# Kernel tuning notes

Measured on AMD Instinct MI355X. Metric: run time of the kernel, lower is better.

Reference implementation:

```python
import jax, jax.numpy as jnp
import numpy as np
import itertools

# ---- module constants (mirroring HyperLayer init) ----
B = 16          # batchsize
K = 16384       # number of learned index tuples (k)
ADD = 32        # additional sampled integer tuples per point
RANK = 2        # len(learn_cols) = w_rank; learn_cols = (0, 1)
P = 2 ** RANK + ADD  # candidate integer tuples per real-valued point
IN_DIM = 65536
OUT_DIM = 65536
EPSILON = 1e-6
SIGMA_BOOST = 2.0

# floor/ceil mask: rows of itertools.product([True, False], repeat=RANK) -> (2^RANK, RANK)
_FLOOR_MASK = jnp.array(
    [[int(b) for b in bools] for bools in itertools.product([True, False], repeat=RANK)],
    dtype=bool,
)


def setup_inputs() -> dict:
    key = jax.random.key(0)
    k1, k2, k3, k4 = jax.random.split(key, 4)
    return {
        "x": jax.random.normal(k1, (B, IN_DIM), jnp.float32),
        "res": jax.random.normal(k2, (B, K, RANK + 2), jnp.float32),
        "bias": jax.random.normal(k3, (OUT_DIM,), jnp.float32),
        "temp_indices": jax.random.randint(k4, (K, 2), 0, IN_DIM, dtype=jnp.int64),
    }


def _forward(x, res, bias, temp_indices):
    bsz = x.shape[0]
    # subrange = [out_size, in_size] for learn_cols = (0, 1)
    size = jnp.array([OUT_DIM, IN_DIM], jnp.float32)

    # ---- split_out: means in [0, size-1], sigmas softplus-scaled by size ----
    means = jax.nn.sigmoid(res[..., :RANK]) * (size - 1.0)               # (B, K, 2)
    sigmas = (jax.nn.softplus(res[..., RANK] + SIGMA_BOOST) + EPSILON)[..., None] * size  # (B, K, 2)
    values = res[..., RANK + 1]                                          # (B, K)

    # ---- discretize: 2^RANK floor/ceil neighbors (on detached means) ----
    m_det = jax.lax.stop_gradient(means)[:, :, None, :]                  # (B, K, 1, 2)
    nb = jnp.where(_FLOOR_MASK[None, None], jnp.floor(m_det), jnp.ceil(m_det)).astype(jnp.int32)  # (B,K,4,2)

    # additional uniformly sampled integer tuples (fixed internal key, deterministic)
    u = jax.random.uniform(jax.random.key(42), (bsz, K, ADD, RANK), jnp.float32) * (1.0 - EPSILON)
    samp = jnp.floor(u * size).astype(jnp.int32)                         # (B, K, ADD, 2)

    ints = jnp.concatenate([nb, samp], axis=2)                           # (B, K, P, 2)
    ints_fl = ints.astype(jnp.float32)

    # diagonal-Gaussian densities of integer tuples under (means, sigmas)
    z = (ints_fl - means[:, :, None, :]) / sigmas[:, :, None, :]         # (B, K, P, 2)
    props = jnp.exp(-0.5 * jnp.sum(z * z, axis=-1))                      # (B, K, P)
    props = props / jnp.sum(props + EPSILON, axis=2, keepdims=True)

    vals = (values[:, :, None] * props).reshape(bsz, -1)                 # (B, L)
    idx = ints.reshape(bsz, -1, RANK)                                    # (B, L, 2)

    # template: hardwired temp_indices, with learn_cols overwritten by discretized indices
    template = jnp.broadcast_to(
        temp_indices.astype(jnp.int32)[None, :, None, :], (bsz, K, P, 2)
    ).reshape(bsz, -1, 2)
    template = template.at[:, :, jnp.array([0, 1])].set(idx)

    out_idx = template[..., 0]                                           # (B, L) in [0, OUT_DIM)
    in_idx = template[..., 1]                                            # (B, L) in [0, IN_DIM)

    # sparse matrix-vector product per batch element: gather then scatter-add
    gathered = jnp.take_along_axis(x, in_idx, axis=1)                    # (B, L)
    contrib = vals * gathered                                            # (B, L)
    flat = (jnp.arange(bsz, dtype=jnp.int32)[:, None] * OUT_DIM + out_idx).reshape(-1)
    y = jnp.zeros((bsz * OUT_DIM,), x.dtype).at[flat].add(contrib.reshape(-1))
    return y.reshape(bsz, OUT_DIM) + bias[None, :]


def reference(x, res, bias, temp_indices):
    return _forward(x, res, bias, temp_indices)
```

## Files before the change

### kernel.cpp

```cpp
#include <hip/hip_runtime.h>
#include <stdint.h>
#include <math.h>

#define NB 16
#define NK 16384
#define NADD 32
#define NP 36
#define DIM 65536

#define TPB 512
#define GPB2 32
#define NCH3 4
#define CHW3 16384

typedef float f32x4 __attribute__((ext_vector_type(4)));
typedef float f32x8 __attribute__((ext_vector_type(8)));
typedef unsigned int u32x2 __attribute__((ext_vector_type(2)));
typedef unsigned int u32x4 __attribute__((ext_vector_type(4)));

#define BAR_LGKM() asm volatile("s_waitcnt lgkmcnt(0)\n\ts_barrier" ::: "memory")

__device__ __forceinline__ uint32_t rotl32(uint32_t x, uint32_t r) {
    return (x << r) | (x >> (32u - r));
}

__device__ __forceinline__ uint32_t tf_bits(uint32_t idx) {
    const uint32_t K1 = 42u;
    const uint32_t K2 = 0x1BD11BDAu ^ 42u;
    uint32_t x0 = 0u;
    uint32_t x1 = idx + K1;
#define TF_ROUND(r) { x0 += x1; x1 = rotl32(x1, r); x1 ^= x0; }
#define TF_G(a,b,c,d) TF_ROUND(a) TF_ROUND(b) TF_ROUND(c) TF_ROUND(d)
    TF_G(13,15,26,6)   x0 += K1;  x1 += K2 + 1u;
    TF_G(17,29,16,24)  x0 += K2;  x1 += 2u;
    TF_G(13,15,26,6)              x1 += K1 + 3u;
    TF_G(17,29,16,24)  x0 += K1;  x1 += K2 + 4u;
    TF_G(13,15,26,6)   x0 += K2;  x1 += 5u;
#undef TF_G
#undef TF_ROUND
    return x0 ^ x1;
}

__device__ __forceinline__ void tf_bits4(uint32_t base,
                                         uint32_t& r0, uint32_t& r1,
                                         uint32_t& r2, uint32_t& r3) {
    const uint32_t K1 = 42u;
    const uint32_t K2 = 0x1BD11BDAu ^ 42u;
    uint32_t x0[4] = {0u, 0u, 0u, 0u};
    uint32_t x1[4] = {base + K1, base + 1u + K1, base + 2u + K1, base + 3u + K1};
#define TFR4(r) { \
    x0[0]+=x1[0]; x1[0]=rotl32(x1[0],r); x1[0]^=x0[0]; \
    x0[1]+=x1[1]; x1[1]=rotl32(x1[1],r); x1[1]^=x0[1]; \
    x0[2]+=x1[2]; x1[2]=rotl32(x1[2],r); x1[2]^=x0[2]; \
    x0[3]+=x1[3]; x1[3]=rotl32(x1[3],r); x1[3]^=x0[3]; }
#define TFG4(a,b,c,d) TFR4(a) TFR4(b) TFR4(c) TFR4(d)
#define INJ4(da, db) { \
    x0[0]+=(da); x1[0]+=(db); x0[1]+=(da); x1[1]+=(db); \
    x0[2]+=(da); x1[2]+=(db); x0[3]+=(da); x1[3]+=(db); }
    TFG4(13,15,26,6)   INJ4(K1, K2 + 1u)
    TFG4(17,29,16,24)  INJ4(K2, 2u)
    TFG4(13,15,26,6)   INJ4(0u, K1 + 3u)
    TFG4(17,29,16,24)  INJ4(K1, K2 + 4u)
    TFG4(13,15,26,6)   INJ4(K2, 5u)
#undef TFR4
#undef TFG4
#undef INJ4
    r0 = x0[0] ^ x1[0];
    r1 = x0[1] ^ x1[1];
    r2 = x0[2] ^ x1[2];
    r3 = x0[3] ^ x1[3];
}

__device__ __forceinline__ float xla_expf(float x0) {
    float x = fminf(fmaxf(x0, -88.3762626647949f), 88.3762626647950f);
    const float fx = floorf(__fadd_rn(__fmul_rn(x, 1.44269504088896341f), 0.5f));
    const float tmp = __fmul_rn(fx, 0.693359375f);
    float z = __fmul_rn(fx, -2.12194440e-4f);
    float r = __fsub_rn(x, tmp);
    r = __fsub_rn(r, z);
    z = __fmul_rn(r, r);
    float y = 1.9875691500E-4f;
    y = __fadd_rn(__fmul_rn(y, r), 1.3981999507E-3f);
    y = __fadd_rn(__fmul_rn(y, r), 8.3334519073E-3f);
    y = __fadd_rn(__fmul_rn(y, r), 4.1665795894E-2f);
    y = __fadd_rn(__fmul_rn(y, r), 1.6666665459E-1f);
    y = __fadd_rn(__fmul_rn(y, r), 5.0000001201E-1f);
    y = __fadd_rn(__fmul_rn(y, z), r);
    y = __fadd_rn(y, 1.0f);
    const int n = (int)fx;
    const float p2n = __uint_as_float((uint32_t)(n + 127) << 23);
    return fmaxf(__fmul_rn(y, p2n), x0);
}

__device__ __forceinline__ uint32_t bf16pair(float a, float b) {
    uint32_t ua = __float_as_uint(a), ub = __float_as_uint(b);
    ua = (ua + 0x7FFFu + ((ua >> 16) & 1u)) >> 16;
    ub = (ub + 0x7FFFu + ((ub >> 16) & 1u)) >> 16;
    return ua | (ub << 16);
}


__global__ __launch_bounds__(TPB, 4) void f1_gen_reduce_bf16(
    const float*  __restrict__ x,
    const float4* __restrict__ res4,
    uint32_t* __restrict__ part)
{
    __shared__ float acc[CHW3];
    f32x4* const acc4 = reinterpret_cast<f32x4*>(acc);
    const int blk = blockIdx.x;
    const uint32_t tid = (uint32_t)blk * TPB + threadIdx.x;
    const int b = (int)(tid >> 14);
    const float* __restrict__ xrow = x + ((size_t)b << 16);

    #pragma unroll
    for (int j = 0; j < 8; ++j)
        acc4[j * TPB + threadIdx.x] = (f32x4)(0.0f);

    const float4 r = res4[tid];

    const float e0 = xla_expf(-r.x);
    const float e1 = xla_expf(-r.y);
    const float s0 = __fdiv_rn(1.0f, __fadd_rn(1.0f, e0));
    const float s1 = __fdiv_rn(1.0f, __fadd_rn(1.0f, e1));
    const float m0 = __fmul_rn(s0, 65535.0f);
    const float m1 = __fmul_rn(s1, 65535.0f);

    const float a2 = r.z + 2.0f;
    const float sp = fmaxf(a2, 0.0f) + log1pf(__expf(-fabsf(a2)));
    const float sigma = (sp + 1e-6f) * 65536.0f;
    const float inv_sig = __builtin_amdgcn_rcpf(sigma);
    const float n2 = -0.5f * inv_sig * inv_sig;
    const float val = r.w;

    uint32_t packed[NP];
    float    xv[NP];

    {
        const float f0 = floorf(m0), c0 = ceilf(m0);
        const float f1v = floorf(m1), c1 = ceilf(m1);
        const uint32_t uf0 = (uint32_t)(int)f0, uc0 = (uint32_t)(int)c0;
        const uint32_t uf1 = (uint32_t)(int)f1v, uc1 = (uint32_t)(int)c1;
        packed[0] = (uf0 << 16) | uf1;  xv[0] = xrow[uf1];
        packed[1] = (uf0 << 16) | uc1;  xv[1] = xrow[uc1];
        packed[2] = (uc0 << 16) | uf1;  xv[2] = xrow[uf1];
        packed[3] = (uc0 << 16) | uc1;  xv[3] = xrow[uc1];
    }

    const float ONE_MEPS = (float)(1.0 - 1e-6);
    const uint32_t base = tid * 64u;
    #pragma unroll
    for (int a = 0; a < NADD; a += 2) {
        uint32_t bb0, bb1, bb2, bb3;
        tf_bits4(base + 2u*(uint32_t)a, bb0, bb1, bb2, bb3);
        const float u0a = __fmul_rn(__uint_as_float((bb0 >> 9) | 0x3f800000u) - 1.0f, ONE_MEPS);
        const float u1a = __fmul_rn(__uint_as_float((bb1 >> 9) | 0x3f800000u) - 1.0f, ONE_MEPS);
        const float s0a = floorf(__fmul_rn(u0a, 65536.0f));
        const float s1a = floorf(__fmul_rn(u1a, 65536.0f));
        const uint32_t pa = ((uint32_t)(int)s0a << 16) | (uint32_t)(int)s1a;
        packed[4 + a] = pa;
        xv[4 + a] = xrow[pa & 0xFFFFu];
        const float u0b = __fmul_rn(__uint_as_float((bb2 >> 9) | 0x3f800000u) - 1.0f, ONE_MEPS);
        const float u1b = __fmul_rn(__uint_as_float((bb3 >> 9) | 0x3f800000u) - 1.0f, ONE_MEPS);
        const float s0b = floorf(__fmul_rn(u0b, 65536.0f));
        const float s1b = floorf(__fmul_rn(u1b, 65536.0f));
        const uint32_t pb = ((uint32_t)(int)s0b << 16) | (uint32_t)(int)s1b;
        packed[5 + a] = pb;
        xv[5 + a] = xrow[pb & 0xFFFFu];
    }

    float w[NP];
    float denom = 0.0f;
    #pragma unroll
    for (int p = 0; p < NP; ++p) {
        const float d0 = (float)(int)(packed[p] >> 16) - m0;
        const float d1 = (float)(int)(packed[p] & 0xFFFFu) - m1;
        const float e = __expf(n2 * fmaf(d1, d1, d0 * d0));
        denom += e + 1e-6f;
        w[p] = e * xv[p];
    }
    const float scale = __fdiv_rn(val, denom);
    #pragma unroll
    for (int p = 0; p < NP; ++p) w[p] *= scale;

    __syncthreads();

    uint32_t* __restrict__ dst = part + ((size_t)blk << 15);
    #pragma unroll 1
    for (uint32_t c = 0; c < NCH3; ++c) {
        #pragma unroll
        for (int p = 0; p < NP; ++p) {
            if ((packed[p] >> 30) == c)
                atomicAdd(&acc[(packed[p] >> 16) & (CHW3 - 1)], w[p]);
        }
        BAR_LGKM();
        u32x2* __restrict__ dst2 =
            reinterpret_cast<u32x2*>(dst + (size_t)c * 8192);
        const bool last = (c == NCH3 - 1);
        #pragma unroll
        for (int j = 0; j < 8; ++j) {
            const int idx = j * TPB + (int)threadIdx.x;
            const f32x4 v = acc4[idx];
            const u32x2 o = { bf16pair(v.x, v.y), bf16pair(v.z, v.w) };
            dst2[idx] = o;
            if (!last) acc4[idx] = (f32x4)(0.0f);
        }
        if (!last) BAR_LGKM();
    }
}

__global__ __launch_bounds__(256) void f2_final_bf16(
    const u32x4* __restrict__ part4,
    const f32x8* __restrict__ bias8,
    f32x8* __restrict__ y8)
{
    const int i = blockIdx.x * 256 + threadIdx.x;
    const int o8 = i & 8191;
    const int b = i >> 13;
    f32x8 s = bias8[o8];
    #pragma unroll
    for (int g = 0; g < GPB2; ++g) {
        const u32x4 p = part4[(((size_t)(b * GPB2 + g)) << 13) + o8];
        s[0] += __uint_as_float(p.x << 16);
        s[1] += __uint_as_float(p.x & 0xFFFF0000u);
        s[2] += __uint_as_float(p.y << 16);
        s[3] += __uint_as_float(p.y & 0xFFFF0000u);
        s[4] += __uint_as_float(p.z << 16);
        s[5] += __uint_as_float(p.z & 0xFFFF0000u);
        s[6] += __uint_as_float(p.w << 16);
        s[7] += __uint_as_float(p.w & 0xFFFF0000u);
    }
    __builtin_nontemporal_store(s, &y8[i]);
}


__device__ __forceinline__ void gen_point(const float4 r, uint32_t tid,
                                          uint32_t* packed, float* w) {
    const float e0 = xla_expf(-r.x);
    const float e1 = xla_expf(-r.y);
    const float s0 = __fdiv_rn(1.0f, __fadd_rn(1.0f, e0));
    const float s1 = __fdiv_rn(1.0f, __fadd_rn(1.0f, e1));
    const float m0 = __fmul_rn(s0, 65535.0f);
    const float m1 = __fmul_rn(s1, 65535.0f);
    const float a2 = r.z + 2.0f;
    const float sp = fmaxf(a2, 0.0f) + log1pf(__expf(-fabsf(a2)));
    const float sigma = (sp + 1e-6f) * 65536.0f;
    const float inv_sig = __builtin_amdgcn_rcpf(sigma);
    const float n2 = -0.5f * inv_sig * inv_sig;
    const float val = r.w;

    const float f0 = floorf(m0), c0 = ceilf(m0);
    const float f1 = floorf(m1), c1 = ceilf(m1);
    {
        const float cd0[4] = {f0, f0, c0, c0};
        const float cd1[4] = {f1, c1, f1, c1};
        #pragma unroll
        for (int p = 0; p < 4; ++p) {
            const float d0 = cd0[p] - m0;
            const float d1 = cd1[p] - m1;
            w[p] = __expf(n2 * fmaf(d1, d1, d0 * d0));
            packed[p] = ((uint32_t)(int)cd0[p] << 16) | (uint32_t)(int)cd1[p];
        }
    }
    const float ONE_MEPS = (float)(1.0 - 1e-6);
    const uint32_t base = tid * 64u;
    #pragma unroll
    for (int a = 0; a < NADD; ++a) {
        const uint32_t bb0 = tf_bits(base + 2u*(uint32_t)a);
        const uint32_t bb1 = tf_bits(base + 2u*(uint32_t)a + 1u);
        const float u0 = __fmul_rn(__uint_as_float((bb0 >> 9) | 0x3f800000u) - 1.0f, ONE_MEPS);
        const float u1 = __fmul_rn(__uint_as_float((bb1 >> 9) | 0x3f800000u) - 1.0f, ONE_MEPS);
        const float s0f = floorf(__fmul_rn(u0, 65536.0f));
        const float s1f = floorf(__fmul_rn(u1, 65536.0f));
        const float d0 = s0f - m0;
        const float d1 = s1f - m1;
        w[4 + a] = __expf(n2 * fmaf(d1, d1, d0 * d0));
        packed[4 + a] = ((uint32_t)(int)s0f << 16) | (uint32_t)(int)s1f;
    }
    float denom = 0.0f;
    #pragma unroll
    for (int p = 0; p < NP; ++p) denom += w[p] + 1e-6f;
    const float scale = __fdiv_rn(val, denom);
    #pragma unroll
    for (int p = 0; p < NP; ++p) w[p] *= scale;
}

__global__ __launch_bounds__(256) void init_bias_kernel(
    const float4* __restrict__ bias4, float4* __restrict__ y4)
{
    const int i = blockIdx.x * 256 + threadIdx.x;
    y4[i] = bias4[i & 16383];
}

__global__ __launch_bounds__(256) void hyper_scatter(
    const float*  __restrict__ x,
    const float4* __restrict__ res4,
    float*        __restrict__ y)
{
    const int tid = blockIdx.x * 256 + threadIdx.x;
    const int b = tid >> 14;
    uint32_t packed[NP];
    float    w[NP];
    gen_point(res4[tid], (uint32_t)tid, packed, w);
    const float* __restrict__ xrow = x + ((size_t)b << 16);
    float*       __restrict__ yrow = y + ((size_t)b << 16);
    #pragma unroll
    for (int p = 0; p < NP; ++p) {
        const float xv = xrow[packed[p] & 0xFFFFu];
        unsafeAtomicAdd(&yrow[packed[p] >> 16], w[p] * xv);
    }
}

extern "C" void kernel_launch(void* const* d_in, const int* in_sizes, int n_in,
                              void* d_out, int out_size, void* d_ws, size_t ws_size,
                              hipStream_t stream) {
    const float*  x     = (const float*)d_in[0];
    const float4* res4  = (const float4*)d_in[1];
    const float4* bias4 = (const float4*)d_in[2];
    float* y = (float*)d_out;

    const size_t need_bf16 = (size_t)NB * GPB2 * DIM * 2;

    if (ws_size >= need_bf16) {
        uint32_t* part = (uint32_t*)d_ws;
        f1_gen_reduce_bf16<<<NB * GPB2, TPB, 0, stream>>>(x, res4, part);
        f2_final_bf16<<<(NB * DIM / 8) / 256, 256, 0, stream>>>(
            (const u32x4*)part, (const f32x8*)bias4, (f32x8*)y);
    } else {
        init_bias_kernel<<<(NB * DIM / 4) / 256, 256, 0, stream>>>(bias4, (float4*)y);
        hyper_scatter<<<(NB * NK) / 256, 256, 0, stream>>>(x, res4, y);
    }
}
```

Measured before the change: 153.5 us.

## Replace LDS-chunked bf16 partial reduction with direct global float atomics

Removes the two-pass scheme, where each block accumulated into shared memory chunks, wrote bf16 partials to workspace and a second kernel summed them with bias. It uses a bias-init kernel followed by a scatter kernel. The scatter kernel reuses the precomputed weighted x values and issues 36 unsafe float atomics per point straight into the output. This drops the large partial-buffer write and read and the bf16 rounding. The cost is heavy global atomic contention across 16K points per batch row.

```diff
diff --git a/kernel.cpp b/kernel.cpp
--- a/kernel.cpp
+++ b/kernel.cpp
@@ -8,17 +8,8 @@
 #define NP 36
 #define DIM 65536
 
-#define TPB 512
-#define GPB2 32
-#define NCH3 4
-#define CHW3 16384
 
 typedef float f32x4 __attribute__((ext_vector_type(4)));
-typedef float f32x8 __attribute__((ext_vector_type(8)));
-typedef unsigned int u32x2 __attribute__((ext_vector_type(2)));
-typedef unsigned int u32x4 __attribute__((ext_vector_type(4)));
-
-#define BAR_LGKM() asm volatile("s_waitcnt lgkmcnt(0)\n\ts_barrier" ::: "memory")
 
 __device__ __forceinline__ uint32_t rotl32(uint32_t x, uint32_t r) {
     return (x << r) | (x >> (32u - r));
@@ -92,29 +83,23 @@
     return fmaxf(__fmul_rn(y, p2n), x0);
 }
 
-__device__ __forceinline__ uint32_t bf16pair(float a, float b) {
-    uint32_t ua = __float_as_uint(a), ub = __float_as_uint(b);
-    ua = (ua + 0x7FFFu + ((ua >> 16) & 1u)) >> 16;
-    ub = (ub + 0x7FFFu + ((ub >> 16) & 1u)) >> 16;
-    return ua | (ub << 16);
+
+__global__ __launch_bounds__(256) void init_bias_kernel(
+    const float4* __restrict__ bias4, float4* __restrict__ y4)
+{
+    const int i = blockIdx.x * 256 + threadIdx.x;
+    y4[i] = bias4[i & 16383];
 }
 
-
-__global__ __launch_bounds__(TPB, 4) void f1_gen_reduce_bf16(
+__global__ __launch_bounds__(256) void hyper_scatter_opt(
     const float*  __restrict__ x,
     const float4* __restrict__ res4,
-    uint32_t* __restrict__ part)
+    float*        __restrict__ y)
 {
-    __shared__ float acc[CHW3];
-    f32x4* const acc4 = reinterpret_cast<f32x4*>(acc);
-    const int blk = blockIdx.x;
-    const uint32_t tid = (uint32_t)blk * TPB + threadIdx.x;
+    const uint32_t tid = (uint32_t)blockIdx.x * 256u + threadIdx.x;
     const int b = (int)(tid >> 14);
     const float* __restrict__ xrow = x + ((size_t)b << 16);
-
-    #pragma unroll
-    for (int j = 0; j < 8; ++j)
-        acc4[j * TPB + threadIdx.x] = (f32x4)(0.0f);
+    float*       __restrict__ yrow = y + ((size_t)b << 16);
 
     const float4 r = res4[tid];
 
@@ -179,134 +164,10 @@
         w[p] = e * xv[p];
     }
     const float scale = __fdiv_rn(val, denom);
-    #pragma unroll
-    for (int p = 0; p < NP; ++p) w[p] *= scale;
 
-    __syncthreads();
-
-    uint32_t* __restrict__ dst = part + ((size_t)blk << 15);
-    #pragma unroll 1
-    for (uint32_t c = 0; c < NCH3; ++c) {
-        #pragma unroll
-        for (int p = 0; p < NP; ++p) {
-            if ((packed[p] >> 30) == c)
-                atomicAdd(&acc[(packed[p] >> 16) & (CHW3 - 1)], w[p]);
-        }
-        BAR_LGKM();
-        u32x2* __restrict__ dst2 =
-            reinterpret_cast<u32x2*>(dst + (size_t)c * 8192);
-        const bool last = (c == NCH3 - 1);
-        #pragma unroll
-        for (int j = 0; j < 8; ++j) {
-            const int idx = j * TPB + (int)threadIdx.x;
-            const f32x4 v = acc4[idx];
-            const u32x2 o = { bf16pair(v.x, v.y), bf16pair(v.z, v.w) };
-            dst2[idx] = o;
-            if (!last) acc4[idx] = (f32x4)(0.0f);
-        }
-        if (!last) BAR_LGKM();
-    }
-}
-
-__global__ __launch_bounds__(256) void f2_final_bf16(
-    const u32x4* __restrict__ part4,
-    const f32x8* __restrict__ bias8,
-    f32x8* __restrict__ y8)
-{
-    const int i = blockIdx.x * 256 + threadIdx.x;
-    const int o8 = i & 8191;
-    const int b = i >> 13;
-    f32x8 s = bias8[o8];
-    #pragma unroll
-    for (int g = 0; g < GPB2; ++g) {
-        const u32x4 p = part4[(((size_t)(b * GPB2 + g)) << 13) + o8];
-        s[0] += __uint_as_float(p.x << 16);
-        s[1] += __uint_as_float(p.x & 0xFFFF0000u);
-        s[2] += __uint_as_float(p.y << 16);
-        s[3] += __uint_as_float(p.y & 0xFFFF0000u);
-        s[4] += __uint_as_float(p.z << 16);
-        s[5] += __uint_as_float(p.z & 0xFFFF0000u);
-        s[6] += __uint_as_float(p.w << 16);
-        s[7] += __uint_as_float(p.w & 0xFFFF0000u);
-    }
-    __builtin_nontemporal_store(s, &y8[i]);
-}
-
-
-__device__ __forceinline__ void gen_point(const float4 r, uint32_t tid,
-                                          uint32_t* packed, float* w) {
-    const float e0 = xla_expf(-r.x);
-    const float e1 = xla_expf(-r.y);
-    const float s0 = __fdiv_rn(1.0f, __fadd_rn(1.0f, e0));
-    const float s1 = __fdiv_rn(1.0f, __fadd_rn(1.0f, e1));
-    const float m0 = __fmul_rn(s0, 65535.0f);
-    const float m1 = __fmul_rn(s1, 65535.0f);
-    const float a2 = r.z + 2.0f;
-    const float sp = fmaxf(a2, 0.0f) + log1pf(__expf(-fabsf(a2)));
-    const float sigma = (sp + 1e-6f) * 65536.0f;
-    const float inv_sig = __builtin_amdgcn_rcpf(sigma);
-    const float n2 = -0.5f * inv_sig * inv_sig;
-    const float val = r.w;
-
-    const float f0 = floorf(m0), c0 = ceilf(m0);
-    const float f1 = floorf(m1), c1 = ceilf(m1);
-    {
-        const float cd0[4] = {f0, f0, c0, c0};
-        const float cd1[4] = {f1, c1, f1, c1};
-        #pragma unroll
-        for (int p = 0; p < 4; ++p) {
-            const float d0 = cd0[p] - m0;
-            const float d1 = cd1[p] - m1;
-            w[p] = __expf(n2 * fmaf(d1, d1, d0 * d0));
-            packed[p] = ((uint32_t)(int)cd0[p] << 16) | (uint32_t)(int)cd1[p];
-        }
-    }
-    const float ONE_MEPS = (float)(1.0 - 1e-6);
-    const uint32_t base = tid * 64u;
-    #pragma unroll
-    for (int a = 0; a < NADD; ++a) {
-        const uint32_t bb0 = tf_bits(base + 2u*(uint32_t)a);
-        const uint32_t bb1 = tf_bits(base + 2u*(uint32_t)a + 1u);
-        const float u0 = __fmul_rn(__uint_as_float((bb0 >> 9) | 0x3f800000u) - 1.0f, ONE_MEPS);
-        const float u1 = __fmul_rn(__uint_as_float((bb1 >> 9) | 0x3f800000u) - 1.0f, ONE_MEPS);
-        const float s0f = floorf(__fmul_rn(u0, 65536.0f));
-        const float s1f = floorf(__fmul_rn(u1, 65536.0f));
-        const float d0 = s0f - m0;
-        const float d1 = s1f - m1;
-        w[4 + a] = __expf(n2 * fmaf(d1, d1, d0 * d0));
-        packed[4 + a] = ((uint32_t)(int)s0f << 16) | (uint32_t)(int)s1f;
-    }
-    float denom = 0.0f;
-    #pragma unroll
-    for (int p = 0; p < NP; ++p) denom += w[p] + 1e-6f;
-    const float scale = __fdiv_rn(val, denom);
-    #pragma unroll
-    for (int p = 0; p < NP; ++p) w[p] *= scale;
-}
-
-__global__ __launch_bounds__(256) void init_bias_kernel(
-    const float4* __restrict__ bias4, float4* __restrict__ y4)
-{
-    const int i = blockIdx.x * 256 + threadIdx.x;
-    y4[i] = bias4[i & 16383];
-}
-
-__global__ __launch_bounds__(256) void hyper_scatter(
-    const float*  __restrict__ x,
-    const float4* __restrict__ res4,
-    float*        __restrict__ y)
-{
-    const int tid = blockIdx.x * 256 + threadIdx.x;
-    const int b = tid >> 14;
-    uint32_t packed[NP];
-    float    w[NP];
-    gen_point(res4[tid], (uint32_t)tid, packed, w);
-    const float* __restrict__ xrow = x + ((size_t)b << 16);
-    float*       __restrict__ yrow = y + ((size_t)b << 16);
     #pragma unroll
     for (int p = 0; p < NP; ++p) {
-        const float xv = xrow[packed[p] & 0xFFFFu];
-        unsafeAtomicAdd(&yrow[packed[p] >> 16], w[p] * xv);
+        unsafeAtomicAdd(&yrow[packed[p] >> 16], w[p] * scale);
     }
 }
 
@@ -318,15 +179,9 @@
     const float4* bias4 = (const float4*)d_in[2];
     float* y = (float*)d_out;
 
-    const size_t need_bf16 = (size_t)NB * GPB2 * DIM * 2;
+    (void)d_ws; (void)ws_size;
 
-    if (ws_size >= need_bf16) {
-        uint32_t* part = (uint32_t*)d_ws;
-        f1_gen_reduce_bf16<<<NB * GPB2, TPB, 0, stream>>>(x, res4, part);
-        f2_final_bf16<<<(NB * DIM / 8) / 256, 256, 0, stream>>>(
-            (const u32x4*)part, (const f32x8*)bias4, (f32x8*)y);
-    } else {
-        init_bias_kernel<<<(NB * DIM / 4) / 256, 256, 0, stream>>>(bias4, (float4*)y);
-        hyper_scatter<<<(NB * NK) / 256, 256, 0, stream>>>(x, res4, y);
-    }
+    init_bias_kernel<<<(NB * DIM / 4) / 256, 256, 0, stream>>>(
+        bias4, (float4*)y);
+    hyper_scatter_opt<<<(NB * NK) / 256, 256, 0, stream>>>(x, res4, y);
 }
```

Measured after the change: 529.9 us. +245.1%, slower.

## Split each point's candidates across two threads with shuffle-combined denominator

Applied to the files above, without the earlier changes.

Each real-valued point is now handled by a pair of threads: both compute the shared sigmoid/softplus terms, one also handles the four floor/ceil neighbours, and each generates and processes 16 of the 32 sampled tuples. The two partial softmax denominators are combined with a lane shuffle. Blocks grow to 1024 threads while still covering 512 points, so the shared-memory chunk clears and flushes take half as many iterations per thread. This cuts per-thread register arrays and the serial Threefry/exp chain to raise parallelism, at the cost of duplicated prologue math, divergence between the two halves, and larger blocks.

```diff
diff --git a/kernel.cpp b/kernel.cpp
--- a/kernel.cpp
+++ b/kernel.cpp
@@ -8,10 +8,12 @@
 #define NP 36
 #define DIM 65536
 
-#define TPB 512
+#define TPB 1024
+#define PPB 512
 #define GPB2 32
 #define NCH3 4
 #define CHW3 16384
+#define NSPT 16
 
 typedef float f32x4 __attribute__((ext_vector_type(4)));
 typedef float f32x8 __attribute__((ext_vector_type(8)));
@@ -108,15 +110,16 @@
     __shared__ float acc[CHW3];
     f32x4* const acc4 = reinterpret_cast<f32x4*>(acc);
     const int blk = blockIdx.x;
-    const uint32_t tid = (uint32_t)blk * TPB + threadIdx.x;
-    const int b = (int)(tid >> 14);
+    const uint32_t half = threadIdx.x & 1u;
+    const uint32_t pid  = (uint32_t)blk * PPB + (threadIdx.x >> 1);
+    const int b = (int)(pid >> 14);
     const float* __restrict__ xrow = x + ((size_t)b << 16);
 
     #pragma unroll
-    for (int j = 0; j < 8; ++j)
+    for (int j = 0; j < 4; ++j)
         acc4[j * TPB + threadIdx.x] = (f32x4)(0.0f);
 
-    const float4 r = res4[tid];
+    const float4 r = res4[pid];
 
     const float e0 = xla_expf(-r.x);
     const float e1 = xla_expf(-r.y);
@@ -132,72 +135,98 @@
     const float n2 = -0.5f * inv_sig * inv_sig;
     const float val = r.w;
 
-    uint32_t packed[NP];
-    float    xv[NP];
-
-    {
+    uint32_t packed_c[4];
+    float    xv_c[4];
+    if (half == 0u) {
         const float f0 = floorf(m0), c0 = ceilf(m0);
         const float f1v = floorf(m1), c1 = ceilf(m1);
         const uint32_t uf0 = (uint32_t)(int)f0, uc0 = (uint32_t)(int)c0;
         const uint32_t uf1 = (uint32_t)(int)f1v, uc1 = (uint32_t)(int)c1;
-        packed[0] = (uf0 << 16) | uf1;  xv[0] = xrow[uf1];
-        packed[1] = (uf0 << 16) | uc1;  xv[1] = xrow[uc1];
-        packed[2] = (uc0 << 16) | uf1;  xv[2] = xrow[uf1];
-        packed[3] = (uc0 << 16) | uc1;  xv[3] = xrow[uc1];
-    }
-
+        packed_c[0] = (uf0 << 16) | uf1;  xv_c[0] = xrow[uf1];
+        packed_c[1] = (uf0 << 16) | uc1;  xv_c[1] = xrow[uc1];
+        packed_c[2] = (uc0 << 16) | uf1;  xv_c[2] = xrow[uf1];
+        packed_c[3] = (uc0 << 16) | uc1;  xv_c[3] = xrow[uc1];
+    }
+
+    uint32_t packed_s[NSPT];
+    float    xv_s[NSPT];
     const float ONE_MEPS = (float)(1.0 - 1e-6);
-    const uint32_t base = tid * 64u;
-    #pragma unroll
-    for (int a = 0; a < NADD; a += 2) {
+    const uint32_t base = pid * 64u + (half << 5);
+    #pragma unroll
+    for (int aa = 0; aa < NSPT; aa += 2) {
         uint32_t bb0, bb1, bb2, bb3;
-        tf_bits4(base + 2u*(uint32_t)a, bb0, bb1, bb2, bb3);
+        tf_bits4(base + 2u*(uint32_t)aa, bb0, bb1, bb2, bb3);
         const float u0a = __fmul_rn(__uint_as_float((bb0 >> 9) | 0x3f800000u) - 1.0f, ONE_MEPS);
         const float u1a = __fmul_rn(__uint_as_float((bb1 >> 9) | 0x3f800000u) - 1.0f, ONE_MEPS);
         const float s0a = floorf(__fmul_rn(u0a, 65536.0f));
         const float s1a = floorf(__fmul_rn(u1a, 65536.0f));
         const uint32_t pa = ((uint32_t)(int)s0a << 16) | (uint32_t)(int)s1a;
-        packed[4 + a] = pa;
-        xv[4 + a] = xrow[pa & 0xFFFFu];
+        packed_s[aa] = pa;
+        xv_s[aa] = xrow[pa & 0xFFFFu];
         const float u0b = __fmul_rn(__uint_as_float((bb2 >> 9) | 0x3f800000u) - 1.0f, ONE_MEPS);
         const float u1b = __fmul_rn(__uint_as_float((bb3 >> 9) | 0x3f800000u) - 1.0f, ONE_MEPS);
         const float s0b = floorf(__fmul_rn(u0b, 65536.0f));
         const float s1b = floorf(__fmul_rn(u1b, 65536.0f));
         const uint32_t pb = ((uint32_t)(int)s0b << 16) | (uint32_t)(int)s1b;
-        packed[5 + a] = pb;
-        xv[5 + a] = xrow[pb & 0xFFFFu];
-    }
-
-    float w[NP];
-    float denom = 0.0f;
-    #pragma unroll
-    for (int p = 0; p < NP; ++p) {
-        const float d0 = (float)(int)(packed[p] >> 16) - m0;
-        const float d1 = (float)(int)(packed[p] & 0xFFFFu) - m1;
+        packed_s[aa + 1] = pb;
+        xv_s[aa + 1] = xrow[pb & 0xFFFFu];
+    }
+
+    float w_c[4];
+    float w_s[NSPT];
+    float d_own = 0.0f;
+    if (half == 0u) {
+        #pragma unroll
+        for (int p = 0; p < 4; ++p) {
+            const float d0 = (float)(int)(packed_c[p] >> 16) - m0;
+            const float d1 = (float)(int)(packed_c[p] & 0xFFFFu) - m1;
+            const float e = __expf(n2 * fmaf(d1, d1, d0 * d0));
+            d_own += e + 1e-6f;
+            w_c[p] = e * xv_c[p];
+        }
+    }
+    #pragma unroll
+    for (int p = 0; p < NSPT; ++p) {
+        const float d0 = (float)(int)(packed_s[p] >> 16) - m0;
+        const float d1 = (float)(int)(packed_s[p] & 0xFFFFu) - m1;
         const float e = __expf(n2 * fmaf(d1, d1, d0 * d0));
-        denom += e + 1e-6f;
-        w[p] = e * xv[p];
-    }
+        d_own += e + 1e-6f;
+        w_s[p] = e * xv_s[p];
+    }
+    const float d_oth = __shfl_xor(d_own, 1, 64);
+    const float denom = (half == 0u) ? __fadd_rn(d_own, d_oth)
+                                     : __fadd_rn(d_oth, d_own);
     const float scale = __fdiv_rn(val, denom);
-    #pragma unroll
-    for (int p = 0; p < NP; ++p) w[p] *= scale;
+    if (half == 0u) {
+        #pragma unroll
+        for (int p = 0; p < 4; ++p) w_c[p] *= scale;
+    }
+    #pragma unroll
+    for (int p = 0; p < NSPT; ++p) w_s[p] *= scale;
 
     __syncthreads();
 
     uint32_t* __restrict__ dst = part + ((size_t)blk << 15);
     #pragma unroll 1
     for (uint32_t c = 0; c < NCH3; ++c) {
-        #pragma unroll
-        for (int p = 0; p < NP; ++p) {
-            if ((packed[p] >> 30) == c)
-                atomicAdd(&acc[(packed[p] >> 16) & (CHW3 - 1)], w[p]);
+        if (half == 0u) {
+            #pragma unroll
+            for (int p = 0; p < 4; ++p) {
+                if ((packed_c[p] >> 30) == c)
+                    atomicAdd(&acc[(packed_c[p] >> 16) & (CHW3 - 1)], w_c[p]);
+            }
+        }
+        #pragma unroll
+        for (int p = 0; p < NSPT; ++p) {
+            if ((packed_s[p] >> 30) == c)
+                atomicAdd(&acc[(packed_s[p] >> 16) & (CHW3 - 1)], w_s[p]);
         }
         BAR_LGKM();
         u32x2* __restrict__ dst2 =
             reinterpret_cast<u32x2*>(dst + (size_t)c * 8192);
         const bool last = (c == NCH3 - 1);
         #pragma unroll
-        for (int j = 0; j < 8; ++j) {
+        for (int j = 0; j < 4; ++j) {
             const int idx = j * TPB + (int)threadIdx.x;
             const f32x4 v = acc4[idx];
             const u32x2 o = { bf16pair(v.x, v.y), bf16pair(v.z, v.w) };
```

Result: slower. 173.6 us (+13.0%).

## Split random sample generation into a separate high-parallelism pre-kernel

Applied to the files above, without the earlier changes.

Adds a kernel that runs the threefry sample generation with one thread per sample pair, filling the whole GPU instead of only the 512 blocks used by the main kernel. The packed integer samples are written to workspace, and the main gather/reduce kernel reads them back with coalesced loads instead of computing them inline. This trades the PRNG compute, which is serialized per thread in a low-occupancy kernel, for one extra launch plus 32 MB of workspace writes and reads. The old fused path is kept as a fallback when the workspace is too small.

```diff
diff --git a/kernel.cpp b/kernel.cpp
--- a/kernel.cpp
+++ b/kernel.cpp
@@ -7,6 +7,7 @@
 #define NADD 32
 #define NP 36
 #define DIM 65536
+#define NPTS (NB * NK)
 
 #define TPB 512
 #define GPB2 32
@@ -99,10 +100,33 @@
     return ua | (ub << 16);
 }
 
-
-__global__ __launch_bounds__(TPB, 4) void f1_gen_reduce_bf16(
+__global__ __launch_bounds__(256) void f0_samples(uint32_t* __restrict__ spack)
+{
+    const uint32_t g = (uint32_t)blockIdx.x * 256u + threadIdx.x;
+    const uint32_t pair  = g >> 18;
+    const uint32_t point = g & (NPTS - 1u);
+    const uint32_t a = pair << 1;
+    uint32_t bb0, bb1, bb2, bb3;
+    tf_bits4(point * 64u + (a << 1), bb0, bb1, bb2, bb3);
+    const float ONE_MEPS = (float)(1.0 - 1e-6);
+    const float u0a = __fmul_rn(__uint_as_float((bb0 >> 9) | 0x3f800000u) - 1.0f, ONE_MEPS);
+    const float u1a = __fmul_rn(__uint_as_float((bb1 >> 9) | 0x3f800000u) - 1.0f, ONE_MEPS);
+    const float s0a = floorf(__fmul_rn(u0a, 65536.0f));
+    const float s1a = floorf(__fmul_rn(u1a, 65536.0f));
+    spack[a * (uint32_t)NPTS + point] =
+        ((uint32_t)(int)s0a << 16) | (uint32_t)(int)s1a;
+    const float u0b = __fmul_rn(__uint_as_float((bb2 >> 9) | 0x3f800000u) - 1.0f, ONE_MEPS);
+    const float u1b = __fmul_rn(__uint_as_float((bb3 >> 9) | 0x3f800000u) - 1.0f, ONE_MEPS);
+    const float s0b = floorf(__fmul_rn(u0b, 65536.0f));
+    const float s1b = floorf(__fmul_rn(u1b, 65536.0f));
+    spack[(a + 1u) * (uint32_t)NPTS + point] =
+        ((uint32_t)(int)s0b << 16) | (uint32_t)(int)s1b;
+}
+
+__global__ __launch_bounds__(TPB, 4) void f1_gen_reduce_pre(
     const float*  __restrict__ x,
     const float4* __restrict__ res4,
+    const uint32_t* __restrict__ spack,
     uint32_t* __restrict__ part)
 {
     __shared__ float acc[CHW3];
@@ -134,7 +158,6 @@
 
     uint32_t packed[NP];
     float    xv[NP];
-
     {
         const float f0 = floorf(m0), c0 = ceilf(m0);
         const float f1v = floorf(m1), c1 = ceilf(m1);
@@ -145,27 +168,11 @@
         packed[2] = (uc0 << 16) | uf1;  xv[2] = xrow[uf1];
         packed[3] = (uc0 << 16) | uc1;  xv[3] = xrow[uc1];
     }
-
-    const float ONE_MEPS = (float)(1.0 - 1e-6);
-    const uint32_t base = tid * 64u;
-    #pragma unroll
-    for (int a = 0; a < NADD; a += 2) {
-        uint32_t bb0, bb1, bb2, bb3;
-        tf_bits4(base + 2u*(uint32_t)a, bb0, bb1, bb2, bb3);
-        const float u0a = __fmul_rn(__uint_as_float((bb0 >> 9) | 0x3f800000u) - 1.0f, ONE_MEPS);
-        const float u1a = __fmul_rn(__uint_as_float((bb1 >> 9) | 0x3f800000u) - 1.0f, ONE_MEPS);
-        const float s0a = floorf(__fmul_rn(u0a, 65536.0f));
-        const float s1a = floorf(__fmul_rn(u1a, 65536.0f));
-        const uint32_t pa = ((uint32_t)(int)s0a << 16) | (uint32_t)(int)s1a;
-        packed[4 + a] = pa;
-        xv[4 + a] = xrow[pa & 0xFFFFu];
-        const float u0b = __fmul_rn(__uint_as_float((bb2 >> 9) | 0x3f800000u) - 1.0f, ONE_MEPS);
-        const float u1b = __fmul_rn(__uint_as_float((bb3 >> 9) | 0x3f800000u) - 1.0f, ONE_MEPS);
-        const float s0b = floorf(__fmul_rn(u0b, 65536.0f));
-        const float s1b = floorf(__fmul_rn(u1b, 65536.0f));
-        const uint32_t pb = ((uint32_t)(int)s0b << 16) | (uint32_t)(int)s1b;
-        packed[5 + a] = pb;
-        xv[5 + a] = xrow[pb & 0xFFFFu];
+    #pragma unroll
+    for (int a = 0; a < NADD; ++a) {
+        const uint32_t pi = spack[(uint32_t)a * (uint32_t)NPTS + tid];
+        packed[4 + a] = pi;
+        xv[4 + a] = xrow[pi & 0xFFFFu];
     }
 
     float w[NP];
@@ -208,6 +215,112 @@
     }
 }
 
+__global__ __launch_bounds__(TPB, 4) void f1_gen_reduce_bf16(
+    const float*  __restrict__ x,
+    const float4* __restrict__ res4,
+    uint32_t* __restrict__ part)
+{
+    __shared__ float acc[CHW3];
+    f32x4* const acc4 = reinterpret_cast<f32x4*>(acc);
+    const int blk = blockIdx.x;
+    const uint32_t tid = (uint32_t)blk * TPB + threadIdx.x;
+    const int b = (int)(tid >> 14);
+    const float* __restrict__ xrow = x + ((size_t)b << 16);
+
+    #pragma unroll
+    for (int j = 0; j < 8; ++j)
+        acc4[j * TPB + threadIdx.x] = (f32x4)(0.0f);
+
+    const float4 r = res4[tid];
+
+    const float e0 = xla_expf(-r.x);
+    const float e1 = xla_expf(-r.y);
+    const float s0 = __fdiv_rn(1.0f, __fadd_rn(1.0f, e0));
+    const float s1 = __fdiv_rn(1.0f, __fadd_rn(1.0f, e1));
+    const float m0 = __fmul_rn(s0, 65535.0f);
+    const float m1 = __fmul_rn(s1, 65535.0f);
+
+    const float a2 = r.z + 2.0f;
+    const float sp = fmaxf(a2, 0.0f) + log1pf(__expf(-fabsf(a2)));
+    const float sigma = (sp + 1e-6f) * 65536.0f;
+    const float inv_sig = __builtin_amdgcn_rcpf(sigma);
+    const float n2 = -0.5f * inv_sig * inv_sig;
+    const float val = r.w;
+
+    uint32_t packed[NP];
+    float    xv[NP];
+    {
+        const float f0 = floorf(m0), c0 = ceilf(m0);
+        const float f1v = floorf(m1), c1 = ceilf(m1);
+        const uint32_t uf0 = (uint32_t)(int)f0, uc0 = (uint32_t)(int)c0;
+        const uint32_t uf1 = (uint32_t)(int)f1v, uc1 = (uint32_t)(int)c1;
+        packed[0] = (uf0 << 16) | uf1;  xv[0] = xrow[uf1];
+        packed[1] = (uf0 << 16) | uc1;  xv[1] = xrow[uc1];
+        packed[2] = (uc0 << 16) | uf1;  xv[2] = xrow[uf1];
+        packed[3] = (uc0 << 16) | uc1;  xv[3] = xrow[uc1];
+    }
+    const float ONE_MEPS = (float)(1.0 - 1e-6);
+    const uint32_t base = tid * 64u;
+    #pragma unroll
+    for (int a = 0; a < NADD; a += 2) {
+        uint32_t bb0, bb1, bb2, bb3;
+        tf_bits4(base + 2u*(uint32_t)a, bb0, bb1, bb2, bb3);
+        const float u0a = __fmul_rn(__uint_as_float((bb0 >> 9) | 0x3f800000u) - 1.0f, ONE_MEPS);
+        const float u1a = __fmul_rn(__uint_as_float((bb1 >> 9) | 0x3f800000u) - 1.0f, ONE_MEPS);
+        const float s0a = floorf(__fmul_rn(u0a, 65536.0f));
+        const float s1a = floorf(__fmul_rn(u1a, 65536.0f));
+        const uint32_t pa = ((uint32_t)(int)s0a << 16) | (uint32_t)(int)s1a;
+        packed[4 + a] = pa;
+        xv[4 + a] = xrow[pa & 0xFFFFu];
+        const float u0b = __fmul_rn(__uint_as_float((bb2 >> 9) | 0x3f800000u) - 1.0f, ONE_MEPS);
+        const float u1b = __fmul_rn(__uint_as_float((bb3 >> 9) | 0x3f800000u) - 1.0f, ONE_MEPS);
+        const float s0b = floorf(__fmul_rn(u0b, 65536.0f));
+        const float s1b = floorf(__fmul_rn(u1b, 65536.0f));
+        const uint32_t pb = ((uint32_t)(int)s0b << 16) | (uint32_t)(int)s1b;
+        packed[5 + a] = pb;
+        xv[5 + a] = xrow[pb & 0xFFFFu];
+    }
+
+    float w[NP];
+    float denom = 0.0f;
+    #pragma unroll
+    for (int p = 0; p < NP; ++p) {
+        const float d0 = (float)(int)(packed[p] >> 16) - m0;
+        const float d1 = (float)(int)(packed[p] & 0xFFFFu) - m1;
+        const float e = __expf(n2 * fmaf(d1, d1, d0 * d0));
+        denom += e + 1e-6f;
+        w[p] = e * xv[p];
+    }
+    const float scale = __fdiv_rn(val, denom);
+    #pragma unroll
+    for (int p = 0; p < NP; ++p) w[p] *= scale;
+
+    __syncthreads();
+
+    uint32_t* __restrict__ dst = part + ((size_t)blk << 15);
+    #pragma unroll 1
+    for (uint32_t c = 0; c < NCH3; ++c) {
+        #pragma unroll
+        for (int p = 0; p < NP; ++p) {
+            if ((packed[p] >> 30) == c)
+                atomicAdd(&acc[(packed[p] >> 16) & (CHW3 - 1)], w[p]);
+        }
+        BAR_LGKM();
+        u32x2* __restrict__ dst2 =
+            reinterpret_cast<u32x2*>(dst + (size_t)c * 8192);
+        const bool last = (c == NCH3 - 1);
+        #pragma unroll
+        for (int j = 0; j < 8; ++j) {
+            const int idx = j * TPB + (int)threadIdx.x;
+            const f32x4 v = acc4[idx];
+            const u32x2 o = { bf16pair(v.x, v.y), bf16pair(v.z, v.w) };
+            dst2[idx] = o;
+            if (!last) acc4[idx] = (f32x4)(0.0f);
+        }
+        if (!last) BAR_LGKM();
+    }
+}
+
 __global__ __launch_bounds__(256) void f2_final_bf16(
     const u32x4* __restrict__ part4,
     const f32x8* __restrict__ bias8,
@@ -319,8 +432,16 @@
     float* y = (float*)d_out;
 
     const size_t need_bf16 = (size_t)NB * GPB2 * DIM * 2;
-
-    if (ws_size >= need_bf16) {
+    const size_t need_pre  = need_bf16 + (size_t)NADD * NPTS * 4;
+
+    if (ws_size >= need_pre) {
+        uint32_t* part  = (uint32_t*)d_ws;
+        uint32_t* spack = (uint32_t*)((char*)d_ws + need_bf16);
+        f0_samples<<<(NADD / 2 * NPTS) / 256, 256, 0, stream>>>(spack);
+        f1_gen_reduce_pre<<<NB * GPB2, TPB, 0, stream>>>(x, res4, spack, part);
+        f2_final_bf16<<<(NB * DIM / 8) / 256, 256, 0, stream>>>(
+            (const u32x4*)part, (const f32x8*)bias4, (f32x8*)y);
+    } else if (ws_size >= need_bf16) {
         uint32_t* part = (uint32_t*)d_ws;
         f1_gen_reduce_bf16<<<NB * GPB2, TPB, 0, stream>>>(x, res4, part);
         f2_final_bf16<<<(NB * DIM / 8) / 256, 256, 0, stream>>>(
```

Result: slower. 185.8 us (+21.0%).
